# Optimization experiments

Measured on AMD Instinct MI355X. Metric: run time of the kernel, lower is better.

The kernel has to match this reference:

```python
import jax, jax.numpy as jnp
import numpy as np

AVG_STEP_WEIGHTING = 0.002


def _mean_rbf_kernel(a, b):
    """Mean over all (i,j) of exp(-||a_i - b_j||^2 / 2), features flattened.

    Equivalent to the original per-row loop: (1/N) * sum_i mean_j k(b, a_i).
    Uses the Gram trick to avoid materializing (N, M, D) intermediates.
    """
    A = a.reshape(a.shape[0], -1)  # (N, D)
    B = b.reshape(b.shape[0], -1)  # (M, D)
    sq_a = jnp.sum(A * A, axis=1)  # (N,)
    sq_b = jnp.sum(B * B, axis=1)  # (M,)
    # (N, M) pairwise squared distances; clamp tiny negatives from fp error
    d2 = jnp.maximum(sq_a[:, None] + sq_b[None, :] - 2.0 * (A @ B.T), 0.0)
    return jnp.mean(jnp.exp(-0.5 * d2))


def setup_inputs() -> dict:
    key = jax.random.key(0)
    kx, ky = jax.random.split(key)
    N, M, D1, D2 = 4096, 4096, 24, 8
    x = jax.random.normal(kx, (N, D1, D2), dtype=jnp.float32)
    y = jax.random.normal(ky, (M, D1, D2), dtype=jnp.float32)
    avg_step = jnp.asarray(5.0, dtype=jnp.float32)
    return {"x": x, "y": y, "avg_step": avg_step}


def reference(x, y, avg_step):
    XX = _mean_rbf_kernel(x, x)
    XY = _mean_rbf_kernel(x, y)
    YY = _mean_rbf_kernel(y, y)
    mmd = XX + YY - 2.0 * XY
    loss = mmd + (jnp.maximum(jnp.asarray(1.0, x.dtype), avg_step) - 1.0) * AVG_STEP_WEIGHTING
    return (loss, mmd)
```

## Files before the change

### kernel.cpp

```cpp
#include <hip/hip_runtime.h>
#include <hip/hip_bf16.h>

typedef __attribute__((ext_vector_type(8))) short short8;
typedef __attribute__((ext_vector_type(4))) float float4v;

#define N_ROWS 4096
#define K_DIM  192
#define NT     32
#define NXX    272
#define NBLK   1056
#define STRE   104
#define STAGE_BYTES (384 * STRE * 2)
#define LDS_TOTAL   (2 * STAGE_BYTES + 32)
#define C1     (-0.72134752044448179f)
#define LOG2E  (1.4426950408889634f)

__global__ void prep_kernel(const float* __restrict__ x, const float* __restrict__ y,
                            __hip_bfloat16* __restrict__ xb, __hip_bfloat16* __restrict__ yb,
                            float* __restrict__ sqx, float* __restrict__ sqy)
{
    int w    = (blockIdx.x * blockDim.x + threadIdx.x) >> 6;
    int lane = threadIdx.x & 63;
    if (w >= 2 * N_ROWS) return;
    const float*      src = (w < N_ROWS) ? (x + (size_t)w * K_DIM) : (y + (size_t)(w - N_ROWS) * K_DIM);
    __hip_bfloat16*   dst = (w < N_ROWS) ? (xb + (size_t)w * K_DIM) : (yb + (size_t)(w - N_ROWS) * K_DIM);
    float s = 0.f;
    #pragma unroll
    for (int i = 0; i < 3; ++i) {
        float f = src[lane + 64 * i];
        __hip_bfloat16 h = __float2bfloat16(f);
        dst[lane + 64 * i] = h;
        float fb = __bfloat162float(h);
        s += fb * fb;
    }
    #pragma unroll
    for (int off = 32; off; off >>= 1) s += __shfl_down(s, off, 64);
    if (lane == 0) {
        if (w < N_ROWS) sqx[w] = s; else sqy[w - N_ROWS] = s;
    }
}

extern __shared__ char smem[];

__global__ __launch_bounds__(512, 2)
void gram_kernel(const __hip_bfloat16* __restrict__ xb, const __hip_bfloat16* __restrict__ yb,
                 const float* __restrict__ sqx, const float* __restrict__ sqy,
                 float* __restrict__ partials)
{
    const short* xbs = (const short*)xb;
    const short* ybs = (const short*)yb;

    int id = blockIdx.x;
    const short *A, *B; const float *sa, *sb;
    int bi, bj0, ntiles, sym;
    if (id < 2 * NXX) {
        int t;
        if (id < NXX) { t = id;       A = xbs; B = xbs; sa = sqx; sb = sqx; }
        else          { t = id - NXX; A = ybs; B = ybs; sa = sqy; sb = sqy; }
        bi = 0;
        for (;;) { int nb = (33 - bi) >> 1; if (t < nb) break; t -= nb; ++bi; }
        bj0 = bi + 2 * t;
        ntiles = (bj0 + 1 < NT) ? 2 : 1;
        sym = 1;
    } else {
        int t = id - 2 * NXX;
        bi = t >> 4; bj0 = (t & 15) * 2; ntiles = 2;
        A = xbs; B = ybs; sa = sqx; sb = sqy; sym = 0;
    }
    const int abase = bi * 128, bbase = bj0 * 128;

    const int tid  = threadIdx.x;
    const int lane = tid & 63, w = tid >> 6;
    const int wm   = w >> 2,  wn = w & 3;
    const int m15  = lane & 15, quad = lane >> 4;

    const short* gsrc[9];
    int ldst[9];
    #pragma unroll
    for (int i = 0; i < 9; ++i) {
        int c   = tid + 512 * i;
        int row = (c * 10923) >> 17;
        int cw  = c - row * 12;
        const short* P; int gr;
        if (row < 128) { P = A; gr = abase + row; }
        else           { P = B; gr = bbase + row - 128; if (gr > N_ROWS - 1) gr = N_ROWS - 1; }
        gsrc[i] = P + (size_t)gr * K_DIM + cw * 8;
        ldst[i] = row * (STRE * 2) + cw * 16;
    }

    uint4 v0[9];
    #pragma unroll
    for (int i = 0; i < 9; ++i) v0[i] = *(const uint4*)(gsrc[i]);

    float4v ua[4]; float vb4[4];
    #pragma unroll
    for (int tm = 0; tm < 4; ++tm)
        ua[tm] = (*(const float4v*)&sa[abase + wm * 64 + tm * 16 + quad * 4]) * C1;
    #pragma unroll
    for (int tn = 0; tn < 4; ++tn) {
        int ci = bbase + wn * 64 + tn * 16 + m15;
        if (ci > N_ROWS - 1) ci = N_ROWS - 1;
        vb4[tn] = C1 * sb[ci];
    }

    float weight = 1.0f;
    if (sym) {
        int sub = wn >> 1;
        weight = (sub >= ntiles) ? 0.0f : (((bj0 + sub) == bi) ? 1.0f : 2.0f);
    }

    #pragma unroll
    for (int i = 0; i < 9; ++i) *(uint4*)(smem + ldst[i]) = v0[i];
    __syncthreads();

    uint4 v1[9];
    #pragma unroll
    for (int i = 0; i < 9; ++i) v1[i] = *(const uint4*)(gsrc[i] + 96);

    int offA[4], offB[4];
    #pragma unroll
    for (int tm = 0; tm < 4; ++tm)
        offA[tm] = (wm * 64 + tm * 16 + m15) * (STRE * 2) + quad * 16;
    #pragma unroll
    for (int tn = 0; tn < 4; ++tn)
        offB[tn] = (128 + wn * 64 + tn * 16 + m15) * (STRE * 2) + quad * 16;

    float4v acc[4][4];
    #pragma unroll
    for (int i = 0; i < 4; ++i)
        #pragma unroll
        for (int j = 0; j < 4; ++j) acc[i][j] = (float4v){0.f, 0.f, 0.f, 0.f};

    #pragma unroll
    for (int ks = 0; ks < 3; ++ks) {
        short8 af[4], bfr[4];
        #pragma unroll
        for (int tm = 0; tm < 4; ++tm) af[tm]  = *(const short8*)(smem + offA[tm] + ks * 64);
        #pragma unroll
        for (int tn = 0; tn < 4; ++tn) bfr[tn] = *(const short8*)(smem + offB[tn] + ks * 64);
        #pragma unroll
        for (int tm = 0; tm < 4; ++tm)
            #pragma unroll
            for (int tn = 0; tn < 4; ++tn)
                acc[tm][tn] = __builtin_amdgcn_mfma_f32_16x16x32_bf16(af[tm], bfr[tn], acc[tm][tn], 0, 0, 0);
    }

    #pragma unroll
    for (int i = 0; i < 9; ++i) *(uint4*)(smem + STAGE_BYTES + ldst[i]) = v1[i];
    __syncthreads();

    #pragma unroll
    for (int ks = 0; ks < 3; ++ks) {
        short8 af[4], bfr[4];
        #pragma unroll
        for (int tm = 0; tm < 4; ++tm) af[tm]  = *(const short8*)(smem + STAGE_BYTES + offA[tm] + ks * 64);
        #pragma unroll
        for (int tn = 0; tn < 4; ++tn) bfr[tn] = *(const short8*)(smem + STAGE_BYTES + offB[tn] + ks * 64);
        #pragma unroll
        for (int tm = 0; tm < 4; ++tm)
            #pragma unroll
            for (int tn = 0; tn < 4; ++tn)
                acc[tm][tn] = __builtin_amdgcn_mfma_f32_16x16x32_bf16(af[tm], bfr[tn], acc[tm][tn], 0, 0, 0);
    }

    float lsum = 0.f;
    #pragma unroll
    for (int tm = 0; tm < 4; ++tm)
        #pragma unroll
        for (int tn = 0; tn < 4; ++tn) {
            float vv = vb4[tn];
            float s0 = fminf(ua[tm][0] + vv + LOG2E * acc[tm][tn][0], 0.f);
            float s1 = fminf(ua[tm][1] + vv + LOG2E * acc[tm][tn][1], 0.f);
            float s2 = fminf(ua[tm][2] + vv + LOG2E * acc[tm][tn][2], 0.f);
            float s3 = fminf(ua[tm][3] + vv + LOG2E * acc[tm][tn][3], 0.f);
            float mx = fmaxf(fmaxf(s0, s1), fmaxf(s2, s3));
            if (__ballot(mx > -40.f)) {
                lsum += __builtin_amdgcn_exp2f(s0) + __builtin_amdgcn_exp2f(s1)
                      + __builtin_amdgcn_exp2f(s2) + __builtin_amdgcn_exp2f(s3);
            }
        }

    #pragma unroll
    for (int off = 32; off; off >>= 1) lsum += __shfl_down(lsum, off, 64);
    float* wred = (float*)(smem + 2 * STAGE_BYTES);
    if (lane == 0) wred[w] = weight * lsum;
    __syncthreads();
    if (tid == 0) {
        float p = 0.f;
        #pragma unroll
        for (int i = 0; i < 8; ++i) p += wred[i];
        partials[id] = p;
    }
}

__global__ void final_kernel(const float* __restrict__ partials, const float* __restrict__ avg_step,
                             float* __restrict__ out)
{
    __shared__ float red[3][4];
    int tid = threadIdx.x, lane = tid & 63, w = tid >> 6;
    float s0 = 0.f, s1 = 0.f, s2 = 0.f;
    for (int i = tid; i < NXX; i += 256) s0 += partials[i];
    for (int i = tid; i < NXX; i += 256) s1 += partials[NXX + i];
    for (int i = tid; i < 512; i += 256) s2 += partials[2 * NXX + i];
    #pragma unroll
    for (int off = 32; off; off >>= 1) {
        s0 += __shfl_down(s0, off, 64);
        s1 += __shfl_down(s1, off, 64);
        s2 += __shfl_down(s2, off, 64);
    }
    if (lane == 0) { red[0][w] = s0; red[1][w] = s1; red[2][w] = s2; }
    __syncthreads();
    if (tid == 0) {
        float sxx = red[0][0] + red[0][1] + red[0][2] + red[0][3];
        float syy = red[1][0] + red[1][1] + red[1][2] + red[1][3];
        float sxy = red[2][0] + red[2][1] + red[2][2] + red[2][3];
        const float inv = 1.0f / 16777216.0f;
        float mmd   = (sxx + syy - 2.0f * sxy) * inv;
        float stepv = fmaxf(1.0f, avg_step[0]);
        out[0] = mmd + (stepv - 1.0f) * 0.002f;
        out[1] = mmd;
    }
}

extern "C" void kernel_launch(void* const* d_in, const int* in_sizes, int n_in,
                              void* d_out, int out_size, void* d_ws, size_t ws_size,
                              hipStream_t stream)
{
    const float* x        = (const float*)d_in[0];
    const float* y        = (const float*)d_in[1];
    const float* avg_step = (const float*)d_in[2];

    char* ws = (char*)d_ws;
    __hip_bfloat16* xb       = (__hip_bfloat16*)(ws);
    __hip_bfloat16* yb       = (__hip_bfloat16*)(ws + 1572864);
    float*          sqx      = (float*)(ws + 3145728);
    float*          sqy      = (float*)(ws + 3162112);
    float*          partials = (float*)(ws + 3178496);

    hipFuncSetAttribute(reinterpret_cast<const void*>(gram_kernel),
                        hipFuncAttributeMaxDynamicSharedMemorySize, LDS_TOTAL);

    prep_kernel<<<2048, 256, 0, stream>>>(x, y, xb, yb, sqx, sqy);
    gram_kernel<<<NBLK, 512, LDS_TOTAL, stream>>>(xb, yb, sqx, sqy, partials);
    final_kernel<<<1, 256, 0, stream>>>(partials, avg_step, (float*)d_out);
}
```

Before: 96.33 us.

## Convert gram kernel to persistent blocks with cross-tile prefetch pipelining

```diff
diff --git a/kernel.cpp b/kernel.cpp
--- a/kernel.cpp
+++ b/kernel.cpp
@@ -6,12 +6,11 @@
 
 #define N_ROWS 4096
 #define K_DIM  192
-#define NT     32
-#define NXX    272
-#define NBLK   1056
-#define STRE   104
-#define STAGE_BYTES (384 * STRE * 2)
-#define LDS_TOTAL   (2 * STAGE_BYTES + 32)
+#define NTILE  1056
+#define GRID_P 256
+#define STRB   208
+#define STG    79872
+#define LDS_TOTAL (2 * STG + 64)
 #define C1     (-0.72134752044448179f)
 #define LOG2E  (1.4426950408889634f)
 
@@ -40,182 +39,186 @@
     }
 }
 
+struct TileMeta {
+    const short* A; const short* B; const float* sa; const float* sb;
+    int ab, bb; float wgt;
+};
+
+__device__ __forceinline__ TileMeta tile_meta(int id, const short* xbs, const short* ybs,
+                                              const float* sqx, const float* sqy, int wm)
+{
+    TileMeta m; int cls, t, bi2, bj;
+    if (id < 544) {
+        if (id < 272) { cls = 0; t = id; } else { cls = 1; t = id - 272; }
+        bi2 = 0;
+        for (;;) { int nb = 32 - 2 * bi2; if (t < nb) break; t -= nb; ++bi2; }
+        bj = 2 * bi2 + t;
+    } else { cls = 2; t = id - 544; bi2 = t >> 5; bj = t & 31; }
+    if (cls == 0)      { m.A = xbs; m.B = xbs; m.sa = sqx; m.sb = sqx; }
+    else if (cls == 1) { m.A = ybs; m.B = ybs; m.sa = sqy; m.sb = sqy; }
+    else               { m.A = xbs; m.B = ybs; m.sa = sqx; m.sb = sqy; }
+    m.ab = bi2 * 256; m.bb = bj * 128;
+    if (cls < 2) {
+        int r128 = 2 * bi2 + (wm >> 1);
+        m.wgt = (bj < r128) ? 0.0f : ((bj == r128) ? 1.0f : 2.0f);
+    } else m.wgt = -2.0f;
+    return m;
+}
+
 extern __shared__ char smem[];
 
 __global__ __launch_bounds__(512, 2)
-void gram_kernel(const __hip_bfloat16* __restrict__ xb, const __hip_bfloat16* __restrict__ yb,
-                 const float* __restrict__ sqx, const float* __restrict__ sqy,
-                 float* __restrict__ partials)
-{
-    const short* xbs = (const short*)xb;
-    const short* ybs = (const short*)yb;
-
-    int id = blockIdx.x;
-    const short *A, *B; const float *sa, *sb;
-    int bi, bj0, ntiles, sym;
-    if (id < 2 * NXX) {
-        int t;
-        if (id < NXX) { t = id;       A = xbs; B = xbs; sa = sqx; sb = sqx; }
-        else          { t = id - NXX; A = ybs; B = ybs; sa = sqy; sb = sqy; }
-        bi = 0;
-        for (;;) { int nb = (33 - bi) >> 1; if (t < nb) break; t -= nb; ++bi; }
-        bj0 = bi + 2 * t;
-        ntiles = (bj0 + 1 < NT) ? 2 : 1;
-        sym = 1;
-    } else {
-        int t = id - 2 * NXX;
-        bi = t >> 4; bj0 = (t & 15) * 2; ntiles = 2;
-        A = xbs; B = ybs; sa = sqx; sb = sqy; sym = 0;
-    }
-    const int abase = bi * 128, bbase = bj0 * 128;
-
-    const int tid  = threadIdx.x;
-    const int lane = tid & 63, w = tid >> 6;
-    const int wm   = w >> 2,  wn = w & 3;
+void gram_persist(const __hip_bfloat16* __restrict__ xb_, const __hip_bfloat16* __restrict__ yb_,
+                  const float* __restrict__ sqx, const float* __restrict__ sqy,
+                  float* __restrict__ partials)
+{
+    const short* xbs = (const short*)xb_;
+    const short* ybs = (const short*)yb_;
+    const int tid  = threadIdx.x, lane = tid & 63, w = tid >> 6;
+    const int wm   = w & 3, wn = w >> 2;
     const int m15  = lane & 15, quad = lane >> 4;
 
-    const short* gsrc[9];
-    int ldst[9];
+    int rel[9], isB[9], loff[9];
     #pragma unroll
     for (int i = 0; i < 9; ++i) {
         int c   = tid + 512 * i;
         int row = (c * 10923) >> 17;
         int cw  = c - row * 12;
-        const short* P; int gr;
-        if (row < 128) { P = A; gr = abase + row; }
-        else           { P = B; gr = bbase + row - 128; if (gr > N_ROWS - 1) gr = N_ROWS - 1; }
-        gsrc[i] = P + (size_t)gr * K_DIM + cw * 8;
-        ldst[i] = row * (STRE * 2) + cw * 16;
-    }
-
-    uint4 v0[9];
-    #pragma unroll
-    for (int i = 0; i < 9; ++i) v0[i] = *(const uint4*)(gsrc[i]);
-
-    float4v ua[4]; float vb4[4];
-    #pragma unroll
-    for (int tm = 0; tm < 4; ++tm)
-        ua[tm] = (*(const float4v*)&sa[abase + wm * 64 + tm * 16 + quad * 4]) * C1;
-    #pragma unroll
-    for (int tn = 0; tn < 4; ++tn) {
-        int ci = bbase + wn * 64 + tn * 16 + m15;
-        if (ci > N_ROWS - 1) ci = N_ROWS - 1;
-        vb4[tn] = C1 * sb[ci];
-    }
-
-    float weight = 1.0f;
-    if (sym) {
-        int sub = wn >> 1;
-        weight = (sub >= ntiles) ? 0.0f : (((bj0 + sub) == bi) ? 1.0f : 2.0f);
-    }
-
-    #pragma unroll
-    for (int i = 0; i < 9; ++i) *(uint4*)(smem + ldst[i]) = v0[i];
-    __syncthreads();
-
-    uint4 v1[9];
-    #pragma unroll
-    for (int i = 0; i < 9; ++i) v1[i] = *(const uint4*)(gsrc[i] + 96);
-
-    int offA[4], offB[4];
-    #pragma unroll
-    for (int tm = 0; tm < 4; ++tm)
-        offA[tm] = (wm * 64 + tm * 16 + m15) * (STRE * 2) + quad * 16;
-    #pragma unroll
-    for (int tn = 0; tn < 4; ++tn)
-        offB[tn] = (128 + wn * 64 + tn * 16 + m15) * (STRE * 2) + quad * 16;
-
-    float4v acc[4][4];
-    #pragma unroll
-    for (int i = 0; i < 4; ++i)
-        #pragma unroll
-        for (int j = 0; j < 4; ++j) acc[i][j] = (float4v){0.f, 0.f, 0.f, 0.f};
-
-    #pragma unroll
-    for (int ks = 0; ks < 3; ++ks) {
-        short8 af[4], bfr[4];
-        #pragma unroll
-        for (int tm = 0; tm < 4; ++tm) af[tm]  = *(const short8*)(smem + offA[tm] + ks * 64);
-        #pragma unroll
-        for (int tn = 0; tn < 4; ++tn) bfr[tn] = *(const short8*)(smem + offB[tn] + ks * 64);
+        int r2  = (row < 256) ? row : row - 256;
+        rel[i]  = r2 * 384 + cw * 16;
+        isB[i]  = (row >= 256);
+        loff[i] = row * STRB + cw * 16;
+    }
+
+    int rbA[4], rbB[4];
+    #pragma unroll
+    for (int q = 0; q < 4; ++q) {
+        rbA[q] = (wm * 64 + q * 16 + m15) * STRB + quad * 16;
+        rbB[q] = (256 + wn * 64 + q * 16 + m15) * STRB + quad * 16;
+    }
+
+    float total = 0.f;
+    const int tcount = (blockIdx.x < NTILE - 4 * GRID_P) ? 5 : 4;
+
+    TileMeta mt = tile_meta(blockIdx.x, xbs, ybs, sqx, sqy, wm);
+    const char* Ap = (const char*)(mt.A + (size_t)mt.ab * K_DIM);
+    const char* Bp = (const char*)(mt.B + (size_t)mt.bb * K_DIM);
+    uint4 v[9];
+    #pragma unroll
+    for (int i = 0; i < 9; ++i) v[i] = *(const uint4*)((isB[i] ? Bp : Ap) + rel[i]);
+
+    for (int k = 0; k < tcount; ++k) {
+        float4v acc[4][4];
+        #pragma unroll
+        for (int a = 0; a < 4; ++a)
+            #pragma unroll
+            for (int b = 0; b < 4; ++b) acc[a][b] = (float4v){0.f, 0.f, 0.f, 0.f};
+
+        float wgt = mt.wgt;
+        const float* sa = mt.sa; const float* sb = mt.sb;
+        const int ab = mt.ab, bb = mt.bb;
+
+        #pragma unroll
+        for (int i = 0; i < 9; ++i) *(uint4*)(smem + loff[i]) = v[i];
+        __syncthreads();
+        float4v ua[4]; float vb4[4];
         #pragma unroll
         for (int tm = 0; tm < 4; ++tm)
-            #pragma unroll
-            for (int tn = 0; tn < 4; ++tn)
-                acc[tm][tn] = __builtin_amdgcn_mfma_f32_16x16x32_bf16(af[tm], bfr[tn], acc[tm][tn], 0, 0, 0);
-    }
-
-    #pragma unroll
-    for (int i = 0; i < 9; ++i) *(uint4*)(smem + STAGE_BYTES + ldst[i]) = v1[i];
-    __syncthreads();
-
-    #pragma unroll
-    for (int ks = 0; ks < 3; ++ks) {
-        short8 af[4], bfr[4];
-        #pragma unroll
-        for (int tm = 0; tm < 4; ++tm) af[tm]  = *(const short8*)(smem + STAGE_BYTES + offA[tm] + ks * 64);
-        #pragma unroll
-        for (int tn = 0; tn < 4; ++tn) bfr[tn] = *(const short8*)(smem + STAGE_BYTES + offB[tn] + ks * 64);
+            ua[tm] = (*(const float4v*)&sa[ab + wm * 64 + tm * 16 + quad * 4]) * C1;
+        #pragma unroll
+        for (int tn = 0; tn < 4; ++tn)
+            vb4[tn] = C1 * sb[bb + wn * 64 + tn * 16 + m15];
+        #pragma unroll
+        for (int i = 0; i < 9; ++i) v[i] = *(const uint4*)((isB[i] ? Bp : Ap) + rel[i] + 192);
+
+        #pragma unroll
+        for (int ks = 0; ks < 3; ++ks) {
+            short8 af[4], bf[4];
+            #pragma unroll
+            for (int tm = 0; tm < 4; ++tm) af[tm] = *(const short8*)(smem + rbA[tm] + ks * 64);
+            #pragma unroll
+            for (int tn = 0; tn < 4; ++tn) bf[tn] = *(const short8*)(smem + rbB[tn] + ks * 64);
+            #pragma unroll
+            for (int tm = 0; tm < 4; ++tm)
+                #pragma unroll
+                for (int tn = 0; tn < 4; ++tn)
+                    acc[tm][tn] = __builtin_amdgcn_mfma_f32_16x16x32_bf16(af[tm], bf[tn], acc[tm][tn], 0, 0, 0);
+        }
+
+        #pragma unroll
+        for (int i = 0; i < 9; ++i) *(uint4*)(smem + STG + loff[i]) = v[i];
+        bool more = (k + 1 < tcount);
+        if (more) {
+            mt = tile_meta(blockIdx.x + GRID_P * (k + 1), xbs, ybs, sqx, sqy, wm);
+            Ap = (const char*)(mt.A + (size_t)mt.ab * K_DIM);
+            Bp = (const char*)(mt.B + (size_t)mt.bb * K_DIM);
+        }
+        __syncthreads();
+        if (more) {
+            #pragma unroll
+            for (int i = 0; i < 9; ++i) v[i] = *(const uint4*)((isB[i] ? Bp : Ap) + rel[i]);
+        }
+
+        #pragma unroll
+        for (int ks = 0; ks < 3; ++ks) {
+            short8 af[4], bf[4];
+            #pragma unroll
+            for (int tm = 0; tm < 4; ++tm) af[tm] = *(const short8*)(smem + STG + rbA[tm] + ks * 64);
+            #pragma unroll
+            for (int tn = 0; tn < 4; ++tn) bf[tn] = *(const short8*)(smem + STG + rbB[tn] + ks * 64);
+            #pragma unroll
+            for (int tm = 0; tm < 4; ++tm)
+                #pragma unroll
+                for (int tn = 0; tn < 4; ++tn)
+                    acc[tm][tn] = __builtin_amdgcn_mfma_f32_16x16x32_bf16(af[tm], bf[tn], acc[tm][tn], 0, 0, 0);
+        }
+
+        float lsum = 0.f;
         #pragma unroll
         for (int tm = 0; tm < 4; ++tm)
             #pragma unroll
-            for (int tn = 0; tn < 4; ++tn)
-                acc[tm][tn] = __builtin_amdgcn_mfma_f32_16x16x32_bf16(af[tm], bfr[tn], acc[tm][tn], 0, 0, 0);
-    }
-
-    float lsum = 0.f;
-    #pragma unroll
-    for (int tm = 0; tm < 4; ++tm)
-        #pragma unroll
-        for (int tn = 0; tn < 4; ++tn) {
-            float vv = vb4[tn];
-            float s0 = fminf(ua[tm][0] + vv + LOG2E * acc[tm][tn][0], 0.f);
-            float s1 = fminf(ua[tm][1] + vv + LOG2E * acc[tm][tn][1], 0.f);
-            float s2 = fminf(ua[tm][2] + vv + LOG2E * acc[tm][tn][2], 0.f);
-            float s3 = fminf(ua[tm][3] + vv + LOG2E * acc[tm][tn][3], 0.f);
-            float mx = fmaxf(fmaxf(s0, s1), fmaxf(s2, s3));
-            if (__ballot(mx > -40.f)) {
-                lsum += __builtin_amdgcn_exp2f(s0) + __builtin_amdgcn_exp2f(s1)
-                      + __builtin_amdgcn_exp2f(s2) + __builtin_amdgcn_exp2f(s3);
+            for (int tn = 0; tn < 4; ++tn) {
+                float vv = vb4[tn];
+                float s0 = fminf(ua[tm][0] + vv + LOG2E * acc[tm][tn][0], 0.f);
+                float s1 = fminf(ua[tm][1] + vv + LOG2E * acc[tm][tn][1], 0.f);
+                float s2 = fminf(ua[tm][2] + vv + LOG2E * acc[tm][tn][2], 0.f);
+                float s3 = fminf(ua[tm][3] + vv + LOG2E * acc[tm][tn][3], 0.f);
+                float mx = fmaxf(fmaxf(s0, s1), fmaxf(s2, s3));
+                if (__ballot(mx > -40.f)) {
+                    lsum += __builtin_amdgcn_exp2f(s0) + __builtin_amdgcn_exp2f(s1)
+                          + __builtin_amdgcn_exp2f(s2) + __builtin_amdgcn_exp2f(s3);
+                }
             }
-        }
-
-    #pragma unroll
-    for (int off = 32; off; off >>= 1) lsum += __shfl_down(lsum, off, 64);
-    float* wred = (float*)(smem + 2 * STAGE_BYTES);
-    if (lane == 0) wred[w] = weight * lsum;
+        total += wgt * lsum;
+    }
+
+    #pragma unroll
+    for (int off = 32; off; off >>= 1) total += __shfl_down(total, off, 64);
+    float* wred = (float*)(smem + 2 * STG);
+    if (lane == 0) wred[w] = total;
     __syncthreads();
     if (tid == 0) {
         float p = 0.f;
         #pragma unroll
         for (int i = 0; i < 8; ++i) p += wred[i];
-        partials[id] = p;
+        partials[blockIdx.x] = p;
     }
 }
 
 __global__ void final_kernel(const float* __restrict__ partials, const float* __restrict__ avg_step,
                              float* __restrict__ out)
 {
-    __shared__ float red[3][4];
+    __shared__ float red[4];
     int tid = threadIdx.x, lane = tid & 63, w = tid >> 6;
-    float s0 = 0.f, s1 = 0.f, s2 = 0.f;
-    for (int i = tid; i < NXX; i += 256) s0 += partials[i];
-    for (int i = tid; i < NXX; i += 256) s1 += partials[NXX + i];
-    for (int i = tid; i < 512; i += 256) s2 += partials[2 * NXX + i];
-    #pragma unroll
-    for (int off = 32; off; off >>= 1) {
-        s0 += __shfl_down(s0, off, 64);
-        s1 += __shfl_down(s1, off, 64);
-        s2 += __shfl_down(s2, off, 64);
-    }
-    if (lane == 0) { red[0][w] = s0; red[1][w] = s1; red[2][w] = s2; }
+    float s = partials[tid];
+    #pragma unroll
+    for (int off = 32; off; off >>= 1) s += __shfl_down(s, off, 64);
+    if (lane == 0) red[w] = s;
     __syncthreads();
     if (tid == 0) {
-        float sxx = red[0][0] + red[0][1] + red[0][2] + red[0][3];
-        float syy = red[1][0] + red[1][1] + red[1][2] + red[1][3];
-        float sxy = red[2][0] + red[2][1] + red[2][2] + red[2][3];
+        float sum = red[0] + red[1] + red[2] + red[3];
         const float inv = 1.0f / 16777216.0f;
-        float mmd   = (sxx + syy - 2.0f * sxy) * inv;
+        float mmd   = sum * inv;
         float stepv = fmaxf(1.0f, avg_step[0]);
         out[0] = mmd + (stepv - 1.0f) * 0.002f;
         out[1] = mmd;
@@ -237,10 +240,10 @@
     float*          sqy      = (float*)(ws + 3162112);
     float*          partials = (float*)(ws + 3178496);
 
-    hipFuncSetAttribute(reinterpret_cast<const void*>(gram_kernel),
+    hipFuncSetAttribute(reinterpret_cast<const void*>(gram_persist),
                         hipFuncAttributeMaxDynamicSharedMemorySize, LDS_TOTAL);
 
     prep_kernel<<<2048, 256, 0, stream>>>(x, y, xb, yb, sqx, sqy);
-    gram_kernel<<<NBLK, 512, LDS_TOTAL, stream>>>(xb, yb, sqx, sqy, partials);
+    gram_persist<<<GRID_P, 512, LDS_TOTAL, stream>>>(xb, yb, sqx, sqy, partials);
     final_kernel<<<1, 256, 0, stream>>>(partials, avg_step, (float*)d_out);
 }
```

Measured after the change: 125.9 us. +30.7%, slower.
